# Kernel optimization log

Hardware: AMD Instinct MI355X
Metric: run time of the kernel (lower is better)

## Reference

```python
import jax, jax.numpy as jnp
import numpy as np


def _lstm_cell(x_t, h, c, w_ih, w_hh, b):
    # x_t, h, c: [B, 1]; w_ih, w_hh: [4, 1]; b: [4]
    # PyTorch gate order: input, forget, cell(g), output
    gates = x_t @ w_ih.T + h @ w_hh.T + b  # [B, 4]
    i, f, g, o = jnp.split(gates, 4, axis=-1)
    i = jax.nn.sigmoid(i)
    f = jax.nn.sigmoid(f)
    o = jax.nn.sigmoid(o)
    g = jnp.tanh(g)
    c = f * c + i * g
    h = o * jnp.tanh(c)
    return h, c


def setup_inputs() -> dict:
    key = jax.random.key(0)
    ks = jax.random.split(key, 8)
    B, T_IN, STEPS = 32768, 1024, 512
    return {
        "x": jax.random.normal(ks[0], (B, 1, T_IN), dtype=jnp.float32),
        "t": jax.random.normal(ks[1], (B, 1, STEPS), dtype=jnp.float32),
        "h0": jax.random.normal(ks[2], (B, 1), dtype=jnp.float32),
        "c0": jax.random.normal(ks[3], (B, 1), dtype=jnp.float32),
        "w_ih": jax.random.normal(ks[4], (4, 1), dtype=jnp.float32),
        "w_hh": jax.random.normal(ks[5], (4, 1), dtype=jnp.float32),
        "b_ih": jax.random.normal(ks[6], (4,), dtype=jnp.float32) * 0.1,
        "b_hh": jax.random.normal(ks[7], (4,), dtype=jnp.float32) * 0.1,
    }


def reference(x, t, h0, c0, w_ih, w_hh, b_ih, b_hh):
    b = b_ih + b_hh
    # open loop: feed every input timestep through the LSTM cell
    xs = jnp.transpose(x[:, 0, :], (1, 0))[:, :, None]  # [T_in, B, 1]

    def open_step(carry, x_t):
        h, c = carry
        h, c = _lstm_cell(x_t, h, c, w_ih, w_hh, b)
        return (h, c), None

    (h, c), _ = jax.lax.scan(open_step, (h0, c0), xs)

    ts = jnp.transpose(t[:, 0, :], (1, 0))[:, :, None]  # [steps, B, 1]

    def closed_step(carry, _):
        h, c, x_in = carry
        h, c = _lstm_cell(x_in, h, c, w_ih, w_hh, b)
        return (h, c, h), h

    steps = ts.shape[0]
    _, preds = jax.lax.scan(closed_step, (h, c, xs[-1]), None, length=steps)
    # criterion = MSELoss(mean), accumulated per step:
    # sum_t mean_B((pred_t - t_t)^2)
    loss = jnp.sum(jnp.mean((preds - ts) ** 2, axis=(1, 2)))
    # pred_seq is detached numpy in the original -> stop_gradient here
    pred_seq = jax.lax.stop_gradient(jnp.transpose(preds[:, :, 0], (1, 0)))  # [B, steps]
    return loss, pred_seq
```

## Files before the change

### kernel.cpp

```cpp
#include <hip/hip_runtime.h>


#define L2E 1.44269504088896340736f
#define B_TOT 32768
#define T_IN 1024
#define STEPS 512

__device__ __forceinline__ float ex2(float x) { return __builtin_amdgcn_exp2f(x); }
__device__ __forceinline__ float rcp(float x) { return __builtin_amdgcn_rcpf(x); }

struct Consts {
    float Ai, Bi, Ci;
    float Af, Bf, Cf;
    float Ag, Bg, Cg;
    float Ao, Bo, Co;
};

__device__ __forceinline__ void lstm_step(float xv, float& h, float& c, const Consts& K) {
    float zi = fmaf(h, K.Bi, fmaf(xv, K.Ai, K.Ci));
    float zf = fmaf(h, K.Bf, fmaf(xv, K.Af, K.Cf));
    float zg = fmaf(h, K.Bg, fmaf(xv, K.Ag, K.Cg));
    float zo = fmaf(h, K.Bo, fmaf(xv, K.Ao, K.Co));
    float ri = rcp(1.0f + ex2(zi));
    float rf = rcp(1.0f + ex2(zf));
    float rg = rcp(1.0f + ex2(zg));
    float ro = rcp(1.0f + ex2(zo));
    float g  = fmaf(-2.0f, rg, 1.0f);
    c = fmaf(rf, c, ri * g);
    float rc = rcp(1.0f + ex2((2.0f * L2E) * c));
    float tc = fmaf(-2.0f, rc, 1.0f);
    h = ro * tc;
}

__global__ __launch_bounds__(64) void lstm_chain_kernel(
    const float* __restrict__ x, const float* __restrict__ t,
    const float* __restrict__ h0, const float* __restrict__ c0,
    const float* __restrict__ w_ih, const float* __restrict__ w_hh,
    const float* __restrict__ b_ih, const float* __restrict__ b_hh,
    float* __restrict__ out)
{
    const int b = blockIdx.x * 64 + threadIdx.x;

    Consts K;
    {
        float bi = b_ih[0] + b_hh[0], bf = b_ih[1] + b_hh[1];
        float bg = b_ih[2] + b_hh[2], bo = b_ih[3] + b_hh[3];
        K.Ai = -L2E * w_ih[0]; K.Bi = -L2E * w_hh[0]; K.Ci = -L2E * bi;
        K.Af = -L2E * w_ih[1]; K.Bf = -L2E * w_hh[1]; K.Cf = -L2E * bf;
        K.Ag =  2.0f * L2E * w_ih[2]; K.Bg = 2.0f * L2E * w_hh[2]; K.Cg = 2.0f * L2E * bg;
        K.Ao = -L2E * w_ih[3]; K.Bo = -L2E * w_hh[3]; K.Co = -L2E * bo;
    }

    float h = h0[b];
    float c = c0[b];

    const float4* xr = (const float4*)(x + (size_t)b * T_IN);
    float4 buf0 = xr[0];
    float4 buf1 = xr[1];
    #pragma unroll 1
    for (int q = 0; q < T_IN / 4; ++q) {
        int pf = q + 2; if (pf > T_IN / 4 - 1) pf = T_IN / 4 - 1;
        float4 nxt = xr[pf];
        lstm_step(buf0.x, h, c, K);
        lstm_step(buf0.y, h, c, K);
        lstm_step(buf0.z, h, c, K);
        lstm_step(buf0.w, h, c, K);
        buf0 = buf1;
        buf1 = nxt;
    }
    float xin = buf0.w;

    const float4* tr = (const float4*)(t + (size_t)b * STEPS);
    float* po = out + 1 + (size_t)b * STEPS;
    float lacc = 0.0f;
    float4 t0 = tr[0];
    float4 t1 = tr[1];
    #pragma unroll 1
    for (int q = 0; q < STEPS / 4; ++q) {
        int pf = q + 2; if (pf > STEPS / 4 - 1) pf = STEPS / 4 - 1;
        float4 tn = tr[pf];
        float p0, p1, p2, p3;
        lstm_step(xin, h, c, K); p0 = h; xin = h;
        lstm_step(xin, h, c, K); p1 = h; xin = h;
        lstm_step(xin, h, c, K); p2 = h; xin = h;
        lstm_step(xin, h, c, K); p3 = h; xin = h;
        float d0 = p0 - t0.x, d1 = p1 - t0.y, d2 = p2 - t0.z, d3 = p3 - t0.w;
        lacc = fmaf(d0, d0, lacc);
        lacc = fmaf(d1, d1, lacc);
        lacc = fmaf(d2, d2, lacc);
        lacc = fmaf(d3, d3, lacc);
        po[q * 4 + 0] = p0;
        po[q * 4 + 1] = p1;
        po[q * 4 + 2] = p2;
        po[q * 4 + 3] = p3;
        t0 = t1;
        t1 = tn;
    }

    #pragma unroll
    for (int off = 32; off > 0; off >>= 1)
        lacc += __shfl_down(lacc, off, 64);
    if (threadIdx.x == 0)
        atomicAdd(out, lacc * (1.0f / (float)B_TOT));
}

extern "C" void kernel_launch(void* const* d_in, const int* in_sizes, int n_in,
                              void* d_out, int out_size, void* d_ws, size_t ws_size,
                              hipStream_t stream) {
    const float* x    = (const float*)d_in[0];
    const float* t    = (const float*)d_in[1];
    const float* h0   = (const float*)d_in[2];
    const float* c0   = (const float*)d_in[3];
    const float* w_ih = (const float*)d_in[4];
    const float* w_hh = (const float*)d_in[5];
    const float* b_ih = (const float*)d_in[6];
    const float* b_hh = (const float*)d_in[7];
    float* out = (float*)d_out;

    hipMemsetAsync(out, 0, sizeof(float), stream);

    lstm_chain_kernel<<<B_TOT / 64, 64, 0, stream>>>(
        x, t, h0, c0, w_ih, w_hh, b_ih, b_hh, out);
}
```

Before: 365.4 us.

## Stage x/t tiles through padded LDS for coalesced loads and transposed stores

```diff
diff --git a/kernel.cpp b/kernel.cpp
--- a/kernel.cpp
+++ b/kernel.cpp
@@ -5,18 +5,16 @@
 #define B_TOT 32768
 #define T_IN 1024
 #define STEPS 512
+#define CH 64
+#define PAD 65
 
-__device__ __forceinline__ float ex2(float x) { return __builtin_amdgcn_exp2f(x); }
-__device__ __forceinline__ float rcp(float x) { return __builtin_amdgcn_rcpf(x); }
+__device__ __forceinline__ float ex2(float x){ return __builtin_amdgcn_exp2f(x); }
+__device__ __forceinline__ float rcp(float x){ return __builtin_amdgcn_rcpf(x); }
 
-struct Consts {
-    float Ai, Bi, Ci;
-    float Af, Bf, Cf;
-    float Ag, Bg, Cg;
-    float Ao, Bo, Co;
-};
+struct K8 { float Ai,Bi,Ci, Af,Bf,Cf, Ag,Bg,Cg, Ao,Bo,Co; };
+struct K4 { float Wi,Ci, Wf,Cf, Wg,Cg, Wo,Co; };
 
-__device__ __forceinline__ void lstm_step(float xv, float& h, float& c, const Consts& K) {
+__device__ __forceinline__ void step_open(float xv, float& h, float& c, const K8& K){
     float zi = fmaf(h, K.Bi, fmaf(xv, K.Ai, K.Ci));
     float zf = fmaf(h, K.Bf, fmaf(xv, K.Af, K.Cf));
     float zg = fmaf(h, K.Bg, fmaf(xv, K.Ag, K.Cg));
@@ -28,8 +26,45 @@
     float g  = fmaf(-2.0f, rg, 1.0f);
     c = fmaf(rf, c, ri * g);
     float rc = rcp(1.0f + ex2((2.0f * L2E) * c));
-    float tc = fmaf(-2.0f, rc, 1.0f);
-    h = ro * tc;
+    h = ro * fmaf(-2.0f, rc, 1.0f);
+}
+
+__device__ __forceinline__ void step_closed(float& h, float& c, const K4& K){
+    float zi = fmaf(h, K.Wi, K.Ci);
+    float zf = fmaf(h, K.Wf, K.Cf);
+    float zg = fmaf(h, K.Wg, K.Cg);
+    float zo = fmaf(h, K.Wo, K.Co);
+    float ri = rcp(1.0f + ex2(zi));
+    float rf = rcp(1.0f + ex2(zf));
+    float rg = rcp(1.0f + ex2(zg));
+    float ro = rcp(1.0f + ex2(zo));
+    float g  = fmaf(-2.0f, rg, 1.0f);
+    c = fmaf(rf, c, ri * g);
+    float rc = rcp(1.0f + ex2((2.0f * L2E) * c));
+    h = ro * fmaf(-2.0f, rc, 1.0f);
+}
+
+__device__ __forceinline__ void stage_issue(const float* __restrict__ base,
+                                            int row_stride, int col0, int lane,
+                                            float4* v){
+    const int r_lo = lane >> 4;
+    const int c4   = lane & 15;
+    #pragma unroll
+    for (int j = 0; j < 16; ++j){
+        int r = j * 4 + r_lo;
+        v[j] = *(const float4*)(base + (size_t)r * row_stride + col0 + c4 * 4);
+    }
+}
+__device__ __forceinline__ void stage_write(float* __restrict__ lds, int lane,
+                                            const float4* v){
+    const int r_lo = lane >> 4;
+    const int c4   = lane & 15;
+    #pragma unroll
+    for (int j = 0; j < 16; ++j){
+        int r = j * 4 + r_lo;
+        float* p = lds + r * PAD + c4 * 4;
+        p[0] = v[j].x; p[1] = v[j].y; p[2] = v[j].z; p[3] = v[j].w;
+    }
 }
 
 __global__ __launch_bounds__(64) void lstm_chain_kernel(
@@ -39,9 +74,14 @@
     const float* __restrict__ b_ih, const float* __restrict__ b_hh,
     float* __restrict__ out)
 {
-    const int b = blockIdx.x * 64 + threadIdx.x;
+    __shared__ float sb[2][64 * PAD];
+    __shared__ float pb[64 * PAD];
 
-    Consts K;
+    const int lane = threadIdx.x;
+    const int b0 = blockIdx.x * 64;
+    const int b = b0 + lane;
+
+    K8 K; K4 K2;
     {
         float bi = b_ih[0] + b_hh[0], bf = b_ih[1] + b_hh[1];
         float bg = b_ih[2] + b_hh[2], bo = b_ih[3] + b_hh[3];
@@ -49,58 +89,68 @@
         K.Af = -L2E * w_ih[1]; K.Bf = -L2E * w_hh[1]; K.Cf = -L2E * bf;
         K.Ag =  2.0f * L2E * w_ih[2]; K.Bg = 2.0f * L2E * w_hh[2]; K.Cg = 2.0f * L2E * bg;
         K.Ao = -L2E * w_ih[3]; K.Bo = -L2E * w_hh[3]; K.Co = -L2E * bo;
+        K2.Wi = K.Ai + K.Bi; K2.Ci = K.Ci;
+        K2.Wf = K.Af + K.Bf; K2.Cf = K.Cf;
+        K2.Wg = K.Ag + K.Bg; K2.Cg = K.Cg;
+        K2.Wo = K.Ao + K.Bo; K2.Co = K.Co;
     }
 
     float h = h0[b];
     float c = c0[b];
 
-    const float4* xr = (const float4*)(x + (size_t)b * T_IN);
-    float4 buf0 = xr[0];
-    float4 buf1 = xr[1];
+    const float* xbase = x + (size_t)b0 * T_IN;
+    const float* tbase = t + (size_t)b0 * STEPS;
+
+    {
+        float4 stg[16];
+        stage_issue(xbase, T_IN, 0, lane, stg);
+        stage_write(sb[0], lane, stg);
+    }
     #pragma unroll 1
-    for (int q = 0; q < T_IN / 4; ++q) {
-        int pf = q + 2; if (pf > T_IN / 4 - 1) pf = T_IN / 4 - 1;
-        float4 nxt = xr[pf];
-        lstm_step(buf0.x, h, c, K);
-        lstm_step(buf0.y, h, c, K);
-        lstm_step(buf0.z, h, c, K);
-        lstm_step(buf0.w, h, c, K);
-        buf0 = buf1;
-        buf1 = nxt;
+    for (int k = 0; k < T_IN / CH; ++k){
+        float4 stg2[16];
+        if (k < T_IN / CH - 1) stage_issue(xbase, T_IN, (k + 1) * CH, lane, stg2);
+        const float* xrow = &sb[k & 1][lane * PAD];
+        #pragma unroll 4
+        for (int s = 0; s < CH; ++s){
+            step_open(xrow[s], h, c, K);
+        }
+        if (k < T_IN / CH - 1) stage_write(sb[(k + 1) & 1], lane, stg2);
     }
-    float xin = buf0.w;
+    float xin = sb[(T_IN / CH - 1) & 1][lane * PAD + (CH - 1)];
 
-    const float4* tr = (const float4*)(t + (size_t)b * STEPS);
-    float* po = out + 1 + (size_t)b * STEPS;
+    {
+        float4 stg[16];
+        stage_issue(tbase, STEPS, 0, lane, stg);
+        stage_write(sb[0], lane, stg);
+    }
     float lacc = 0.0f;
-    float4 t0 = tr[0];
-    float4 t1 = tr[1];
     #pragma unroll 1
-    for (int q = 0; q < STEPS / 4; ++q) {
-        int pf = q + 2; if (pf > STEPS / 4 - 1) pf = STEPS / 4 - 1;
-        float4 tn = tr[pf];
-        float p0, p1, p2, p3;
-        lstm_step(xin, h, c, K); p0 = h; xin = h;
-        lstm_step(xin, h, c, K); p1 = h; xin = h;
-        lstm_step(xin, h, c, K); p2 = h; xin = h;
-        lstm_step(xin, h, c, K); p3 = h; xin = h;
-        float d0 = p0 - t0.x, d1 = p1 - t0.y, d2 = p2 - t0.z, d3 = p3 - t0.w;
-        lacc = fmaf(d0, d0, lacc);
-        lacc = fmaf(d1, d1, lacc);
-        lacc = fmaf(d2, d2, lacc);
-        lacc = fmaf(d3, d3, lacc);
-        po[q * 4 + 0] = p0;
-        po[q * 4 + 1] = p1;
-        po[q * 4 + 2] = p2;
-        po[q * 4 + 3] = p3;
-        t0 = t1;
-        t1 = tn;
+    for (int k = 0; k < STEPS / CH; ++k){
+        float4 stg2[16];
+        if (k < STEPS / CH - 1) stage_issue(tbase, STEPS, (k + 1) * CH, lane, stg2);
+        const float* trow = &sb[k & 1][lane * PAD];
+        float* prow = &pb[lane * PAD];
+        #pragma unroll 4
+        for (int s = 0; s < CH; ++s){
+            if (k == 0 && s == 0) step_open(xin, h, c, K);
+            else                  step_closed(h, c, K2);
+            float d = h - trow[s];
+            lacc = fmaf(d, d, lacc);
+            prow[s] = h;
+        }
+        float* obase = out + 1 + (size_t)b0 * STEPS + k * CH + lane;
+        #pragma unroll 4
+        for (int r = 0; r < 64; ++r){
+            obase[(size_t)r * STEPS] = pb[r * PAD + lane];
+        }
+        if (k < STEPS / CH - 1) stage_write(sb[(k + 1) & 1], lane, stg2);
     }
 
     #pragma unroll
     for (int off = 32; off > 0; off >>= 1)
         lacc += __shfl_down(lacc, off, 64);
-    if (threadIdx.x == 0)
+    if (lane == 0)
         atomicAdd(out, lacc * (1.0f / (float)B_TOT));
 }
 
```

Measured after the change: 355.4 us. 1.03x faster.
